# Performance work log

Measured on AMD Instinct MI355X. Metric: run time of the kernel, lower is better.

The kernel has to match this reference:

```python
import jax, jax.numpy as jnp
import numpy as np

HEADS = 2
BN_EPS = 1e-5


def _upsample2x_bilinear_ac(x):
    # torch nn.Upsample(scale_factor=2, mode='bilinear', align_corners=True)
    B, C, H, W = x.shape

    def grid(n):
        c = jnp.arange(2 * n) * ((n - 1) / (2 * n - 1))  # align_corners mapping
        i0 = jnp.clip(jnp.floor(c).astype(jnp.int32), 0, n - 2)
        w = (c - i0).astype(x.dtype)
        return i0, w

    i0, wh = grid(H)
    j0, ww = grid(W)
    x = x[:, :, i0, :] * (1 - wh)[None, None, :, None] + x[:, :, i0 + 1, :] * wh[None, None, :, None]
    x = x[:, :, :, j0] * (1 - ww) + x[:, :, :, j0 + 1] * ww
    return x


def _self_attn(x, wq, wkv, wo, wob):
    # x: (b, t, d); lucidrains axial_attention SelfAttention
    b, t, d = x.shape
    e = d // HEADS
    q = x @ wq
    k, v = jnp.split(x @ wkv, 2, axis=-1)
    mh = lambda z: z.reshape(b, t, HEADS, e).transpose(0, 2, 1, 3)  # (b,h,t,e)
    q, k, v = mh(q), mh(k), mh(v)
    dots = jnp.einsum('bhie,bhje->bhij', q, k) * (e ** -0.5)
    attn = jax.nn.softmax(dots, axis=-1)
    o = jnp.einsum('bhij,bhje->bhie', attn, v)
    o = o.transpose(0, 2, 1, 3).reshape(b, t, d)
    return o @ wo + wob


def setup_inputs() -> dict:
    key = jax.random.key(0)
    ks = jax.random.split(key, 16)
    C, E = 256, 128
    cat = 2 * C + E
    s = 0.02
    inp = {
        'x': jax.random.normal(ks[0], (4, C, 64, 64), jnp.float32),
        'res': jax.random.normal(ks[1], (4, E, 128, 128), jnp.float32),
        'wq_h': jax.random.normal(ks[2], (C, C), jnp.float32) * s,
        'wkv_h': jax.random.normal(ks[3], (C, 2 * C), jnp.float32) * s,
        'wo_h': jax.random.normal(ks[4], (C, C), jnp.float32) * s,
        'wob_h': jnp.zeros((C,), jnp.float32),
        'wq_w': jax.random.normal(ks[5], (C, C), jnp.float32) * s,
        'wkv_w': jax.random.normal(ks[6], (C, 2 * C), jnp.float32) * s,
        'wo_w': jax.random.normal(ks[7], (C, C), jnp.float32) * s,
        'wob_w': jnp.zeros((C,), jnp.float32),
        'conv_w': jax.random.normal(ks[8], (cat, E), jnp.float32) * s,
        'gamma': jnp.ones((E,), jnp.float32),
        'beta': jnp.zeros((E,), jnp.float32),
    }
    return inp


def reference(x, res, wq_h, wkv_h, wo_h, wob_h, wq_w, wkv_w, wo_w, wob_w, conv_w, gamma, beta):
    xu = _upsample2x_bilinear_ac(x)  # (B,C,2H,2W)
    B, C, H, W = xu.shape
    # axial attention along H (rows): batch over B*W
    ah = xu.transpose(0, 3, 2, 1).reshape(B * W, H, C)
    ah = _self_attn(ah, wq_h, wkv_h, wo_h, wob_h).reshape(B, W, H, C).transpose(0, 3, 2, 1)
    # axial attention along W (cols): batch over B*H
    aw = xu.transpose(0, 2, 3, 1).reshape(B * H, W, C)
    aw = _self_attn(aw, wq_w, wkv_w, wo_w, wob_w).reshape(B, H, W, C).transpose(0, 3, 1, 2)
    x_attn = jax.nn.relu(ah + aw)  # sum_axial_out=True, then ReLU
    cat = jnp.concatenate([x_attn, xu, res], axis=1)  # (B, 2C+E, H, W)
    y = jnp.einsum('bchw,ce->behw', cat, conv_w)  # conv1x1, no bias
    y = jax.nn.relu(y)
    # BatchNorm2d, training-mode batch stats (biased variance)
    mu = y.mean(axis=(0, 2, 3), keepdims=True)
    var = y.var(axis=(0, 2, 3), keepdims=True)
    y = (y - mu) / jnp.sqrt(var + BN_EPS)
    return y * gamma[None, :, None, None] + beta[None, :, None, None]
```

## Files before the change

### kernel.cpp

```cpp
#include <hip/hip_runtime.h>
#include <hip/hip_bf16.h>
#include <cstdio>


typedef short bf16x8 __attribute__((ext_vector_type(8)));
typedef short bf16x4 __attribute__((ext_vector_type(4)));
typedef float f32x4 __attribute__((ext_vector_type(4)));

#define MFMA16(a, b, c) __builtin_amdgcn_mfma_f32_16x16x32_bf16((a), (b), (c), 0, 0, 0)

__device__ __forceinline__ short f2bf(float v) {
  __hip_bfloat16 h = __float2bfloat16(v);
  union { __hip_bfloat16 h; short s; } u; u.h = h; return u.s;
}
__device__ __forceinline__ float bf2f(short s) {
  return __uint_as_float(((unsigned int)(unsigned short)s) << 16);
}
__device__ __forceinline__ int swz(int row, int col) {
  return col ^ ((row & 7) << 3);
}

struct WtAll {
  const float* src[7];
  short* dst[7];
  int K[7], N[7], tile0[7];
};

__global__ __launch_bounds__(256) void k_wt_all(WtAll P) {
  const int bid = blockIdx.x;
  int i = 0;
#pragma unroll
  for (int j = 1; j < 7; j++) if (bid >= P.tile0[j]) i = j;
  const float* src = P.src[i];
  short* dst = P.dst[i];
  const int K = P.K[i], N = P.N[i];
  const int local = bid - P.tile0[i];
  const int ktiles = K >> 5;
  const int nt = local / ktiles, kt = local - nt * ktiles;
  const int k0 = kt * 32, n0 = nt * 32;
  __shared__ float tile[32][33];
  const int tx = threadIdx.x & 31, ty = threadIdx.x >> 5;
#pragma unroll
  for (int r = 0; r < 4; r++)
    tile[ty + r * 8][tx] = src[(size_t)(k0 + ty + r * 8) * N + n0 + tx];
  __syncthreads();
#pragma unroll
  for (int r = 0; r < 4; r++)
    dst[(size_t)(n0 + ty + r * 8) * K + k0 + tx] = f2bf(tile[tx][ty + r * 8]);
}

__global__ __launch_bounds__(256) void k_upsample(const float* __restrict__ x,
                                                  short* __restrict__ xu) {
  __shared__ float ldsV[64][65];
  const int bh = blockIdx.x, z = blockIdx.y;
  const int b = bh >> 7, h = bh & 127;
  const float chf = h * (63.0f / 127.0f);
  int i0 = (int)chf; if (i0 > 62) i0 = 62;
  const float wh = chf - (float)i0;
  const int t = threadIdx.x;
  const int cbase = z * 64;
  const float* xb = x + ((size_t)(b * 256 + cbase) * 64 + i0) * 64;
#pragma unroll
  for (int p = 0; p < 16; p++) {
    const int li = p * 256 + t;
    const int c = li >> 6, w = li & 63;
    const float* px = xb + (size_t)c * 4096 + w;
    const float v0 = px[0], v1 = px[64];
    ldsV[c][w] = v0 * (1.f - wh) + v1 * wh;
  }
  __syncthreads();
  const int cg = t & 7, wi = t >> 3;
  short* xout = xu + (size_t)(bh * 128) * 256 + cbase + cg * 8;
#pragma unroll
  for (int p = 0; p < 4; p++) {
    const int w = p * 32 + wi;
    const float cwf = w * (63.0f / 127.0f);
    int j0 = (int)cwf; if (j0 > 62) j0 = 62;
    const float ww = cwf - (float)j0;
    bf16x8 o;
#pragma unroll
    for (int u = 0; u < 8; u++) {
      const float v0 = ldsV[cg * 8 + u][j0], v1 = ldsV[cg * 8 + u][j0 + 1];
      o[u] = f2bf(v0 * (1.f - ww) + v1 * ww);
    }
    *(bf16x8*)(xout + (size_t)w * 256) = o;
  }
}

__global__ __launch_bounds__(512, 2) void k_fused(const short* __restrict__ xu,
                                                  const short* __restrict__ wqkvT0,
                                                  const short* __restrict__ woT0,
                                                  const float* __restrict__ wob0,
                                                  const float* __restrict__ wob1,
                                                  short* __restrict__ accb0,
                                                  short* __restrict__ accb1) {
  __shared__ __align__(16) short Xs[128][256];
  __shared__ __align__(16) short Qb[128][128];
  __shared__ __align__(16) short Kb[128][128];
  __shared__ __align__(16) short Vtb[128][128];

  const int dir = blockIdx.y;
  const short* wqkvT = wqkvT0 + (size_t)dir * 196608;
  const short* woT   = woT0 + (size_t)dir * 65536;
  const float* wob   = dir ? wob1 : wob0;
  short* accb        = dir ? accb1 : accb0;

  const int s = blockIdx.x;
  const int b = s >> 7, pos = s & 127;
  const int tok0 = b * 16384 + (dir ? pos * 128 : pos);
  const int tstep = dir ? 1 : 128;
  const int tid = threadIdx.x;
  const int lane = tid & 63, wid = tid >> 6;
  const int lr = lane & 15, kb = lane >> 4;
  const int ct = wid * 16;
  const float scale = 0.08838834764831845f;

#pragma unroll
  for (int p = 0; p < 8; p++) {
    const int u = p * 512 + tid;
    const int row = u >> 5, ck = (u & 31) * 8;
    bf16x8 v = *(const bf16x8*)(xu + (size_t)(tok0 + row * tstep) * 256 + ck);
    *(bf16x8*)&Xs[row][swz(row, ck)] = v;
  }

  f32x4 accp[2][8];
#pragma unroll
  for (int i = 0; i < 2; i++)
#pragma unroll
    for (int j = 0; j < 8; j++) accp[i][j] = (f32x4){0.f, 0.f, 0.f, 0.f};

  for (int h = 0; h < 2; h++) {
    const short* wqb = wqkvT + (size_t)(h * 128 + ct + lr) * 256 + kb * 8;
    const short* wkb = wqkvT + (size_t)(256 + h * 128 + ct + lr) * 256 + kb * 8;
    const short* wvb = wqkvT + (size_t)(512 + h * 128 + ct + lr) * 256 + kb * 8;
    bf16x8 wq[8], wk[8], wv[8];
#pragma unroll
    for (int ks = 0; ks < 8; ks++) {
      wq[ks] = *(const bf16x8*)(wqb + ks * 32);
      wk[ks] = *(const bf16x8*)(wkb + ks * 32);
      wv[ks] = *(const bf16x8*)(wvb + ks * 32);
    }

    __syncthreads();

#pragma unroll
    for (int nt = 0; nt < 8; nt++) {
      const int xrow = nt * 16 + lr;
      f32x4 dq = (f32x4){0.f, 0.f, 0.f, 0.f};
      f32x4 dk = (f32x4){0.f, 0.f, 0.f, 0.f};
      f32x4 dv = (f32x4){0.f, 0.f, 0.f, 0.f};
#pragma unroll
      for (int ks = 0; ks < 8; ks++) {
        bf16x8 xf = *(const bf16x8*)&Xs[xrow][swz(xrow, kb * 8 + ks * 32)];
        dq = MFMA16(wq[ks], xf, dq);
        dk = MFMA16(wk[ks], xf, dk);
        dv = MFMA16(xf, wv[ks], dv);
      }
      const int trow = nt * 16 + lr, cc = ct + kb * 4;
      bf16x4 pq = {f2bf(dq[0]), f2bf(dq[1]), f2bf(dq[2]), f2bf(dq[3])};
      bf16x4 pk = {f2bf(dk[0]), f2bf(dk[1]), f2bf(dk[2]), f2bf(dk[3])};
      *(bf16x4*)&Qb[trow][swz(trow, cc)] = pq;
      *(bf16x4*)&Kb[trow][swz(trow, cc)] = pk;
      const int vrow = ct + lr;
      bf16x4 pv = {f2bf(dv[0]), f2bf(dv[1]), f2bf(dv[2]), f2bf(dv[3])};
      *(bf16x4*)&Vtb[vrow][swz(vrow, nt * 16 + kb * 4)] = pv;
    }

    __syncthreads();

    f32x4 s8[8];
#pragma unroll
    for (int i = 0; i < 8; i++) s8[i] = (f32x4){0.f, 0.f, 0.f, 0.f};
    const int qrow = ct + lr;
#pragma unroll
    for (int ks = 0; ks < 4; ks++) {
      bf16x8 aq = *(const bf16x8*)&Qb[qrow][swz(qrow, kb * 8 + ks * 32)];
#pragma unroll
      for (int nj = 0; nj < 8; nj++) {
        const int krow = nj * 16 + lr;
        bf16x8 bk = *(const bf16x8*)&Kb[krow][swz(krow, kb * 8 + ks * 32)];
        s8[nj] = MFMA16(bk, aq, s8[nj]);
      }
    }
    {
      float m = s8[0][0];
#pragma unroll
      for (int nj = 0; nj < 8; nj++)
#pragma unroll
        for (int r = 0; r < 4; r++) m = fmaxf(m, s8[nj][r]);
      m = fmaxf(m, __shfl_xor(m, 16));
      m = fmaxf(m, __shfl_xor(m, 32));
      float sum = 0.f;
#pragma unroll
      for (int nj = 0; nj < 8; nj++)
#pragma unroll
        for (int r = 0; r < 4; r++) {
          s8[nj][r] = __expf((s8[nj][r] - m) * scale);
          sum += s8[nj][r];
        }
      sum += __shfl_xor(sum, 16);
      sum += __shfl_xor(sum, 32);
      const float inv = 1.f / sum;
#pragma unroll
      for (int nj = 0; nj < 8; nj++) {
        bf16x4 pp = {f2bf(s8[nj][0] * inv), f2bf(s8[nj][1] * inv),
                     f2bf(s8[nj][2] * inv), f2bf(s8[nj][3] * inv)};
        *(bf16x4*)&Qb[qrow][swz(qrow, nj * 16 + kb * 4)] = pp;
      }
    }

    f32x4 o8[8];
#pragma unroll
    for (int i = 0; i < 8; i++) o8[i] = (f32x4){0.f, 0.f, 0.f, 0.f};
#pragma unroll
    for (int ks = 0; ks < 4; ks++) {
      bf16x8 bp = *(const bf16x8*)&Qb[qrow][swz(qrow, kb * 8 + ks * 32)];
#pragma unroll
      for (int mi = 0; mi < 8; mi++) {
        const int vrow = mi * 16 + lr;
        bf16x8 av = *(const bf16x8*)&Vtb[vrow][swz(vrow, kb * 8 + ks * 32)];
        o8[mi] = MFMA16(av, bp, o8[mi]);
      }
    }

#pragma unroll
    for (int mi = 0; mi < 8; mi++) {
      const int cc = mi * 16 + kb * 4;
      bf16x4 po = {f2bf(o8[mi][0]), f2bf(o8[mi][1]), f2bf(o8[mi][2]), f2bf(o8[mi][3])};
      *(bf16x4*)&Qb[qrow][swz(qrow, cc)] = po;
    }

    __syncthreads();

    {
      const short* w0 = woT + (size_t)(wid * 32 + lr) * 256 + h * 128 + kb * 8;
      const short* w1 = woT + (size_t)(wid * 32 + 16 + lr) * 256 + h * 128 + kb * 8;
      bf16x8 wa[4], wb2[4];
#pragma unroll
      for (int ks = 0; ks < 4; ks++) {
        wa[ks]  = *(const bf16x8*)(w0 + ks * 32);
        wb2[ks] = *(const bf16x8*)(w1 + ks * 32);
      }
#pragma unroll
      for (int nt = 0; nt < 8; nt++) {
        const int trow = nt * 16 + lr;
#pragma unroll
        for (int ks = 0; ks < 4; ks++) {
          bf16x8 bo = *(const bf16x8*)&Qb[trow][swz(trow, kb * 8 + ks * 32)];
          accp[0][nt] = MFMA16(wa[ks], bo, accp[0][nt]);
          accp[1][nt] = MFMA16(wb2[ks], bo, accp[1][nt]);
        }
      }
    }
  }

#pragma unroll
  for (int mi2 = 0; mi2 < 2; mi2++) {
    const int outc = wid * 32 + mi2 * 16 + kb * 4;
    const float b0 = wob[outc], b1 = wob[outc + 1];
    const float b2 = wob[outc + 2], b3 = wob[outc + 3];
#pragma unroll
    for (int nt = 0; nt < 8; nt++) {
      const int token = tok0 + (nt * 16 + lr) * tstep;
      bf16x4 pv = {f2bf(accp[mi2][nt][0] + b0), f2bf(accp[mi2][nt][1] + b1),
                   f2bf(accp[mi2][nt][2] + b2), f2bf(accp[mi2][nt][3] + b3)};
      *(bf16x4*)(accb + (size_t)token * 256 + outc) = pv;
    }
  }
}

__global__ __launch_bounds__(256) void k_gemm_conv(const short* __restrict__ accb0,
                                                   const short* __restrict__ accb1,
                                                   const short* __restrict__ xu,
                                                   const float* __restrict__ res,
                                                   const short* __restrict__ Bt,
                                                   short* __restrict__ ytmp,
                                                   float* __restrict__ partial) {
  __shared__ float redS[2][128], redS2[2][128];
  const int tid = threadIdx.x;
  const int lane = tid & 63, wid = tid >> 6;
  const int lr = lane & 15, kb = lane >> 4;
  const int wr = wid >> 1, wc = wid & 1;
  const int m0 = blockIdx.y * 128;
  f32x4 acc[4][4];
#pragma unroll
  for (int i = 0; i < 4; i++)
#pragma unroll
    for (int j = 0; j < 4; j++) acc[i][j] = (f32x4){0.f, 0.f, 0.f, 0.f};
  const short* arow0 = accb0 + (size_t)(m0 + wr * 64 + lr) * 256 + kb * 8;
  const short* arow1 = accb1 + (size_t)(m0 + wr * 64 + lr) * 256 + kb * 8;
  const short* arow2 = xu + (size_t)(m0 + wr * 64 + lr) * 256 + kb * 8;
  const short* brow = Bt + (size_t)(wc * 64 + lr) * 640 + kb * 8;
#pragma unroll
  for (int ks = 0; ks < 8; ks++) {
    bf16x8 a[4], b[4];
#pragma unroll
    for (int mi = 0; mi < 4; mi++) {
      bf16x8 t0 = *(const bf16x8*)(arow0 + (size_t)mi * 16 * 256 + ks * 32);
      bf16x8 t1 = *(const bf16x8*)(arow1 + (size_t)mi * 16 * 256 + ks * 32);
      bf16x8 tv;
#pragma unroll
      for (int u = 0; u < 8; u++) {
        float sv = bf2f(t0[u]) + bf2f(t1[u]);
        tv[u] = f2bf(fmaxf(sv, 0.f));
      }
      a[mi] = tv;
    }
#pragma unroll
    for (int nj = 0; nj < 4; nj++)
      b[nj] = *(const bf16x8*)(brow + (size_t)nj * 16 * 640 + ks * 32);
#pragma unroll
    for (int mi = 0; mi < 4; mi++)
#pragma unroll
      for (int nj = 0; nj < 4; nj++)
        acc[mi][nj] = MFMA16(a[mi], b[nj], acc[mi][nj]);
  }
#pragma unroll
  for (int ks = 8; ks < 16; ks++) {
    bf16x8 a[4], b[4];
#pragma unroll
    for (int mi = 0; mi < 4; mi++)
      a[mi] = *(const bf16x8*)(arow2 + (size_t)mi * 16 * 256 + (ks - 8) * 32);
#pragma unroll
    for (int nj = 0; nj < 4; nj++)
      b[nj] = *(const bf16x8*)(brow + (size_t)nj * 16 * 640 + ks * 32);
#pragma unroll
    for (int mi = 0; mi < 4; mi++)
#pragma unroll
      for (int nj = 0; nj < 4; nj++)
        acc[mi][nj] = MFMA16(a[mi], b[nj], acc[mi][nj]);
  }
  const int bC = (m0 >> 14) * 128;
  const int hh = (m0 >> 7) & 127;
#pragma unroll
  for (int ks = 16; ks < 20; ks++) {
    const int e0 = (ks - 16) * 32 + kb * 8;
    bf16x8 a[4], b[4];
#pragma unroll
    for (int mi = 0; mi < 4; mi++) {
      const int wl = wr * 64 + mi * 16 + lr;
      const float* rp = res + ((size_t)(bC + e0) * 128 + hh) * 128 + wl;
      bf16x8 tv;
#pragma unroll
      for (int u = 0; u < 8; u++) tv[u] = f2bf(rp[(size_t)u * 16384]);
      a[mi] = tv;
    }
#pragma unroll
    for (int nj = 0; nj < 4; nj++)
      b[nj] = *(const bf16x8*)(brow + (size_t)nj * 16 * 640 + ks * 32);
#pragma unroll
    for (int mi = 0; mi < 4; mi++)
#pragma unroll
      for (int nj = 0; nj < 4; nj++)
        acc[mi][nj] = MFMA16(a[mi], b[nj], acc[mi][nj]);
  }
#pragma unroll
  for (int nj = 0; nj < 4; nj++) {
    float s = 0.f, s2 = 0.f;
    const int c = wc * 64 + nj * 16 + lr;
#pragma unroll
    for (int mi = 0; mi < 4; mi++) {
      const int rbase = m0 + wr * 64 + mi * 16 + kb * 4;
#pragma unroll
      for (int r = 0; r < 4; r++) {
        const float yv = fmaxf(acc[mi][nj][r], 0.f);
        ytmp[(size_t)(rbase + r) * 128 + c] = f2bf(yv);
        s += yv; s2 += yv * yv;
      }
    }
    s += __shfl_xor(s, 16);  s += __shfl_xor(s, 32);
    s2 += __shfl_xor(s2, 16); s2 += __shfl_xor(s2, 32);
    if (kb == 0) { redS[wr][c] = s; redS2[wr][c] = s2; }
  }
  __syncthreads();
  if (tid < 128) {
    partial[((size_t)blockIdx.y * 128 + tid) * 2]     = redS[0][tid] + redS[1][tid];
    partial[((size_t)blockIdx.y * 128 + tid) * 2 + 1] = redS2[0][tid] + redS2[1][tid];
  }
}

__global__ __launch_bounds__(64) void k_bnstats2(const float* __restrict__ partial,
                                                 float* __restrict__ stats) {
  const int ch = blockIdx.x;
  const int t = threadIdx.x;
  float s = 0.f, s2 = 0.f;
  for (int i = t; i < 512; i += 64) {
    s  += partial[(size_t)(i * 128 + ch) * 2];
    s2 += partial[(size_t)(i * 128 + ch) * 2 + 1];
  }
#pragma unroll
  for (int d = 1; d < 64; d <<= 1) {
    s  += __shfl_xor(s, d);
    s2 += __shfl_xor(s2, d);
  }
  if (t == 0) {
    const float mu = s * (1.f / 65536.f);
    const float var = s2 * (1.f / 65536.f) - mu * mu;
    stats[ch * 2] = mu;
    stats[ch * 2 + 1] = rsqrtf(var + 1e-5f);
  }
}

__global__ __launch_bounds__(256) void k_bnout(const short* __restrict__ y,
                                               const float* __restrict__ stats,
                                               const float* __restrict__ gamma,
                                               const float* __restrict__ beta,
                                               float* __restrict__ out) {
  const int bh = blockIdx.x;
  const int b = bh >> 7, h = bh & 127;
  const int w = threadIdx.x & 127, half = threadIdx.x >> 7;
  const short* yp = y + (size_t)(bh * 128 + w) * 128 + half * 64;
  float* op = out + ((size_t)(b * 128) << 14) + h * 128 + w;
#pragma unroll
  for (int e8 = 0; e8 < 8; e8++) {
    bf16x8 v = *(const bf16x8*)(yp + e8 * 8);
#pragma unroll
    for (int u = 0; u < 8; u++) {
      const int e = half * 64 + e8 * 8 + u;
      const float mu = stats[e * 2], rstd = stats[e * 2 + 1];
      op[(size_t)e << 14] = (bf2f(v[u]) - mu) * rstd * gamma[e] + beta[e];
    }
  }
}

extern "C" void kernel_launch(void* const* d_in, const int* in_sizes, int n_in,
                              void* d_out, int out_size, void* d_ws, size_t ws_size,
                              hipStream_t stream) {
  const float* x      = (const float*)d_in[0];
  const float* res    = (const float*)d_in[1];
  const float* wq_h   = (const float*)d_in[2];
  const float* wkv_h  = (const float*)d_in[3];
  const float* wo_h   = (const float*)d_in[4];
  const float* wob_h  = (const float*)d_in[5];
  const float* wq_w   = (const float*)d_in[6];
  const float* wkv_w  = (const float*)d_in[7];
  const float* wo_w   = (const float*)d_in[8];
  const float* wob_w  = (const float*)d_in[9];
  const float* conv_w = (const float*)d_in[10];
  const float* gamma  = (const float*)d_in[11];
  const float* beta   = (const float*)d_in[12];

  char* ws = (char*)d_ws;
  short* wqkvT[2] = {(short*)(ws + 0), (short*)(ws + 393216)};
  short* woT[2]   = {(short*)(ws + 786432), (short*)(ws + 917504)};
  short* convT    = (short*)(ws + 1048576);
  short* xu       = (short*)(ws + 1245184);
  short* ytmp     = (short*)(ws + 34799616);
  float* partial  = (float*)(ws + 51576832);
  float* stats    = (float*)(ws + 52101120);
  short* accb1    = (short*)(ws + 52102144);
  short* accb0    = (short*)d_out;
  float* out      = (float*)d_out;

  if (ws_size < 85656576ull)
    fprintf(stderr, "kernel_launch: ws_size %zu too small\n", ws_size);

  WtAll P;
  P.src[0] = wq_h;  P.dst[0] = wqkvT[0];          P.K[0] = 256; P.N[0] = 256; P.tile0[0] = 0;
  P.src[1] = wkv_h; P.dst[1] = wqkvT[0] + 65536;  P.K[1] = 256; P.N[1] = 512; P.tile0[1] = 64;
  P.src[2] = wq_w;  P.dst[2] = wqkvT[1];          P.K[2] = 256; P.N[2] = 256; P.tile0[2] = 192;
  P.src[3] = wkv_w; P.dst[3] = wqkvT[1] + 65536;  P.K[3] = 256; P.N[3] = 512; P.tile0[3] = 256;
  P.src[4] = wo_h;  P.dst[4] = woT[0];            P.K[4] = 256; P.N[4] = 256; P.tile0[4] = 384;
  P.src[5] = wo_w;  P.dst[5] = woT[1];            P.K[5] = 256; P.N[5] = 256; P.tile0[5] = 448;
  P.src[6] = conv_w;P.dst[6] = convT;             P.K[6] = 640; P.N[6] = 128; P.tile0[6] = 512;
  k_wt_all<<<592, 256, 0, stream>>>(P);

  k_upsample<<<dim3(512, 4), 256, 0, stream>>>(x, xu);

  k_fused<<<dim3(512, 2), 512, 0, stream>>>(xu, wqkvT[0], woT[0],
                                            wob_h, wob_w, accb0, accb1);

  k_gemm_conv<<<dim3(1, 512), 256, 0, stream>>>(accb0, accb1, xu, res, convT,
                                                ytmp, partial);
  k_bnstats2<<<128, 64, 0, stream>>>(partial, stats);
  k_bnout<<<512, 256, 0, stream>>>(ytmp, stats, gamma, beta, out);
}
```

Before: 229.1 us.

## Merge prep kernels and pre-transpose residual to bf16 token-major layout

Folds the weight-transpose and upsample kernels into a single prep launch, and adds a third block range that transposes the residual tensor from channel-major fp32 to token-major bf16 in workspace. The conv GEMM then reads the residual operand with contiguous 16-byte vector loads instead of eight strided scalar fp32 loads per fragment. This removes one launch and makes the residual loads coalesced. The cost is an extra full write and read of the residual (about 16 MB) and a larger workspace requirement.

```diff
diff --git a/kernel.cpp b/kernel.cpp
--- a/kernel.cpp
+++ b/kernel.cpp
@@ -6,6 +6,7 @@
 typedef short bf16x8 __attribute__((ext_vector_type(8)));
 typedef short bf16x4 __attribute__((ext_vector_type(4)));
 typedef float f32x4 __attribute__((ext_vector_type(4)));
+typedef unsigned int u32x4 __attribute__((ext_vector_type(4)));
 
 #define MFMA16(a, b, c) __builtin_amdgcn_mfma_f32_16x16x32_bf16((a), (b), (c), 0, 0, 0)
 
@@ -26,64 +27,95 @@
   int K[7], N[7], tile0[7];
 };
 
-__global__ __launch_bounds__(256) void k_wt_all(WtAll P) {
+__global__ __launch_bounds__(256) void k_prep(WtAll P,
+                                              const float* __restrict__ x,
+                                              short* __restrict__ xu,
+                                              const float* __restrict__ res,
+                                              short* __restrict__ resT) {
+  __shared__ __align__(16) char lbuf[33280];
   const int bid = blockIdx.x;
-  int i = 0;
-#pragma unroll
-  for (int j = 1; j < 7; j++) if (bid >= P.tile0[j]) i = j;
-  const float* src = P.src[i];
-  short* dst = P.dst[i];
-  const int K = P.K[i], N = P.N[i];
-  const int local = bid - P.tile0[i];
-  const int ktiles = K >> 5;
-  const int nt = local / ktiles, kt = local - nt * ktiles;
-  const int k0 = kt * 32, n0 = nt * 32;
-  __shared__ float tile[32][33];
-  const int tx = threadIdx.x & 31, ty = threadIdx.x >> 5;
-#pragma unroll
-  for (int r = 0; r < 4; r++)
-    tile[ty + r * 8][tx] = src[(size_t)(k0 + ty + r * 8) * N + n0 + tx];
-  __syncthreads();
-#pragma unroll
-  for (int r = 0; r < 4; r++)
-    dst[(size_t)(n0 + ty + r * 8) * K + k0 + tx] = f2bf(tile[tx][ty + r * 8]);
-}
-
-__global__ __launch_bounds__(256) void k_upsample(const float* __restrict__ x,
-                                                  short* __restrict__ xu) {
-  __shared__ float ldsV[64][65];
-  const int bh = blockIdx.x, z = blockIdx.y;
-  const int b = bh >> 7, h = bh & 127;
-  const float chf = h * (63.0f / 127.0f);
-  int i0 = (int)chf; if (i0 > 62) i0 = 62;
-  const float wh = chf - (float)i0;
   const int t = threadIdx.x;
-  const int cbase = z * 64;
-  const float* xb = x + ((size_t)(b * 256 + cbase) * 64 + i0) * 64;
-#pragma unroll
-  for (int p = 0; p < 16; p++) {
-    const int li = p * 256 + t;
-    const int c = li >> 6, w = li & 63;
-    const float* px = xb + (size_t)c * 4096 + w;
-    const float v0 = px[0], v1 = px[64];
-    ldsV[c][w] = v0 * (1.f - wh) + v1 * wh;
-  }
-  __syncthreads();
-  const int cg = t & 7, wi = t >> 3;
-  short* xout = xu + (size_t)(bh * 128) * 256 + cbase + cg * 8;
-#pragma unroll
-  for (int p = 0; p < 4; p++) {
-    const int w = p * 32 + wi;
-    const float cwf = w * (63.0f / 127.0f);
-    int j0 = (int)cwf; if (j0 > 62) j0 = 62;
-    const float ww = cwf - (float)j0;
-    bf16x8 o;
-#pragma unroll
-    for (int u = 0; u < 8; u++) {
-      const float v0 = ldsV[cg * 8 + u][j0], v1 = ldsV[cg * 8 + u][j0 + 1];
-      o[u] = f2bf(v0 * (1.f - ww) + v1 * ww);
-    }
-    *(bf16x8*)(xout + (size_t)w * 256) = o;
+
+  if (bid < 592) {
+    float (*tile)[33] = (float(*)[33])lbuf;
+    int i = 0;
+#pragma unroll
+    for (int j = 1; j < 7; j++) if (bid >= P.tile0[j]) i = j;
+    const float* src = P.src[i];
+    short* dst = P.dst[i];
+    const int K = P.K[i], N = P.N[i];
+    const int local = bid - P.tile0[i];
+    const int ktiles = K >> 5;
+    const int nt = local / ktiles, kt = local - nt * ktiles;
+    const int k0 = kt * 32, n0 = nt * 32;
+    const int tx = t & 31, ty = t >> 5;
+#pragma unroll
+    for (int r = 0; r < 4; r++)
+      tile[ty + r * 8][tx] = src[(size_t)(k0 + ty + r * 8) * N + n0 + tx];
+    __syncthreads();
+#pragma unroll
+    for (int r = 0; r < 4; r++)
+      dst[(size_t)(n0 + ty + r * 8) * K + k0 + tx] = f2bf(tile[tx][ty + r * 8]);
+  } else if (bid < 2640) {
+    float (*ldsV)[65] = (float(*)[65])lbuf;
+    const int idx = bid - 592;
+    const int bh = idx >> 2, z = idx & 3;
+    const int b = bh >> 7, h = bh & 127;
+    const float chf = h * (63.0f / 127.0f);
+    int i0 = (int)chf; if (i0 > 62) i0 = 62;
+    const float wh = chf - (float)i0;
+    const int cbase = z * 64;
+    const float* xb = x + ((size_t)(b * 256 + cbase) * 64 + i0) * 64;
+#pragma unroll
+    for (int p = 0; p < 16; p++) {
+      const int li = p * 256 + t;
+      const int c = li >> 6, w = li & 63;
+      const float* px = xb + (size_t)c * 4096 + w;
+      const float v0 = px[0], v1 = px[64];
+      ldsV[c][w] = v0 * (1.f - wh) + v1 * wh;
+    }
+    __syncthreads();
+    const int cg = t & 7, wi = t >> 3;
+    short* xout = xu + (size_t)(bh * 128) * 256 + cbase + cg * 8;
+#pragma unroll
+    for (int p = 0; p < 4; p++) {
+      const int w = p * 32 + wi;
+      const float cwf = w * (63.0f / 127.0f);
+      int j0 = (int)cwf; if (j0 > 62) j0 = 62;
+      const float ww = cwf - (float)j0;
+      bf16x8 o;
+#pragma unroll
+      for (int u = 0; u < 8; u++) {
+        const float v0 = ldsV[cg * 8 + u][j0], v1 = ldsV[cg * 8 + u][j0 + 1];
+        o[u] = f2bf(v0 * (1.f - ww) + v1 * ww);
+      }
+      *(bf16x8*)(xout + (size_t)w * 256) = o;
+    }
+  } else {
+    short (*T)[130] = (short(*)[130])lbuf;
+    const int idx = bid - 2640;
+    const int b = idx >> 7, h = idx & 127;
+    const float* rb = res + (size_t)b * 128 * 16384 + (size_t)h * 128;
+#pragma unroll
+    for (int p = 0; p < 16; p++) {
+      const int li = p * 256 + t;
+      const int e = li >> 5, q = li & 31;
+      f32x4 v = *(const f32x4*)(rb + (size_t)e * 16384 + q * 4);
+#pragma unroll
+      for (int j = 0; j < 4; j++) T[q * 4 + j][e] = f2bf(v[j]);
+    }
+    __syncthreads();
+    short* ob = resT + ((size_t)b * 16384 + (size_t)h * 128) * 128;
+#pragma unroll
+    for (int p = 0; p < 8; p++) {
+      const int li = p * 256 + t;
+      const int w = li >> 4, g = li & 15;
+      union { u32x4 u; bf16x8 v; } cv;
+#pragma unroll
+      for (int j2 = 0; j2 < 4; j2++)
+        cv.u[j2] = *(const unsigned*)&T[w][g * 8 + j2 * 2];
+      *(bf16x8*)(ob + (size_t)w * 128 + g * 8) = cv.v;
+    }
   }
 }
 
@@ -272,7 +304,7 @@
 __global__ __launch_bounds__(256) void k_gemm_conv(const short* __restrict__ accb0,
                                                    const short* __restrict__ accb1,
                                                    const short* __restrict__ xu,
-                                                   const float* __restrict__ res,
+                                                   const short* __restrict__ resT,
                                                    const short* __restrict__ Bt,
                                                    short* __restrict__ ytmp,
                                                    float* __restrict__ partial) {
@@ -290,6 +322,7 @@
   const short* arow0 = accb0 + (size_t)(m0 + wr * 64 + lr) * 256 + kb * 8;
   const short* arow1 = accb1 + (size_t)(m0 + wr * 64 + lr) * 256 + kb * 8;
   const short* arow2 = xu + (size_t)(m0 + wr * 64 + lr) * 256 + kb * 8;
+  const short* arow3 = resT + (size_t)(m0 + wr * 64 + lr) * 128 + kb * 8;
   const short* brow = Bt + (size_t)(wc * 64 + lr) * 640 + kb * 8;
 #pragma unroll
   for (int ks = 0; ks < 8; ks++) {
@@ -330,21 +363,12 @@
       for (int nj = 0; nj < 4; nj++)
         acc[mi][nj] = MFMA16(a[mi], b[nj], acc[mi][nj]);
   }
-  const int bC = (m0 >> 14) * 128;
-  const int hh = (m0 >> 7) & 127;
 #pragma unroll
   for (int ks = 16; ks < 20; ks++) {
-    const int e0 = (ks - 16) * 32 + kb * 8;
     bf16x8 a[4], b[4];
 #pragma unroll
-    for (int mi = 0; mi < 4; mi++) {
-      const int wl = wr * 64 + mi * 16 + lr;
-      const float* rp = res + ((size_t)(bC + e0) * 128 + hh) * 128 + wl;
-      bf16x8 tv;
-#pragma unroll
-      for (int u = 0; u < 8; u++) tv[u] = f2bf(rp[(size_t)u * 16384]);
-      a[mi] = tv;
-    }
+    for (int mi = 0; mi < 4; mi++)
+      a[mi] = *(const bf16x8*)(arow3 + (size_t)mi * 16 * 128 + (ks - 16) * 32);
 #pragma unroll
     for (int nj = 0; nj < 4; nj++)
       b[nj] = *(const bf16x8*)(brow + (size_t)nj * 16 * 640 + ks * 32);
@@ -449,10 +473,11 @@
   float* partial  = (float*)(ws + 51576832);
   float* stats    = (float*)(ws + 52101120);
   short* accb1    = (short*)(ws + 52102144);
+  short* resT     = (short*)(ws + 85656576);
   short* accb0    = (short*)d_out;
   float* out      = (float*)d_out;
 
-  if (ws_size < 85656576ull)
+  if (ws_size < 102433792ull)
     fprintf(stderr, "kernel_launch: ws_size %zu too small\n", ws_size);
 
   WtAll P;
@@ -463,14 +488,12 @@
   P.src[4] = wo_h;  P.dst[4] = woT[0];            P.K[4] = 256; P.N[4] = 256; P.tile0[4] = 384;
   P.src[5] = wo_w;  P.dst[5] = woT[1];            P.K[5] = 256; P.N[5] = 256; P.tile0[5] = 448;
   P.src[6] = conv_w;P.dst[6] = convT;             P.K[6] = 640; P.N[6] = 128; P.tile0[6] = 512;
-  k_wt_all<<<592, 256, 0, stream>>>(P);
-
-  k_upsample<<<dim3(512, 4), 256, 0, stream>>>(x, xu);
+  k_prep<<<3152, 256, 0, stream>>>(P, x, xu, res, resT);
 
   k_fused<<<dim3(512, 2), 512, 0, stream>>>(xu, wqkvT[0], woT[0],
                                             wob_h, wob_w, accb0, accb1);
 
-  k_gemm_conv<<<dim3(1, 512), 256, 0, stream>>>(accb0, accb1, xu, res, convT,
+  k_gemm_conv<<<dim3(1, 512), 256, 0, stream>>>(accb0, accb1, xu, resT, convT,
                                                 ytmp, partial);
   k_bnstats2<<<128, 64, 0, stream>>>(partial, stats);
   k_bnout<<<512, 256, 0, stream>>>(ytmp, stats, gamma, beta, out);
```

New measurement: 229.2 us. No clear change (+0.0%).
